# Performance work log

Hardware: AMD Instinct MI355X
Metric: run time of the kernel (lower is better)

## Reference

```python
import jax, jax.numpy as jnp
import numpy as np

B, S, HID = 8, 1024, 1024
NH, HD = 16, 64  # num heads, head dim
EPS = 1e-12


def setup_inputs() -> dict:
    key = jax.random.key(0)
    ks = jax.random.split(key, 8)
    sc = 0.02
    return {
        "hidden_states": jax.random.normal(ks[0], (B, S, HID), jnp.float32),
        "attention_mask": jnp.zeros((B, 1, 1, S), jnp.bool_),
        "rel_pos": jax.random.normal(ks[1], (1, NH, S, S), jnp.float32),
        "rel_2d_pos": jax.random.normal(ks[2], (1, NH, S, S), jnp.float32),
        "w_qkv": jax.random.normal(ks[3], (3 * HID, HID), jnp.float32) * sc,
        "q_bias": jnp.zeros((1, 1, HID), jnp.float32),
        "v_bias": jnp.zeros((1, 1, HID), jnp.float32),
        "w_out": jax.random.normal(ks[4], (HID, HID), jnp.float32) * sc,
        "b_out": jnp.zeros((HID,), jnp.float32),
        "ln_gamma": jnp.ones((HID,), jnp.float32),
        "ln_beta": jnp.zeros((HID,), jnp.float32),
    }


def reference(hidden_states, attention_mask, rel_pos, rel_2d_pos,
              w_qkv, q_bias, v_bias, w_out, b_out, ln_gamma, ln_beta):
    x = hidden_states
    # fast_qkv: single projection, no bias; then add q_bias/v_bias
    qkv = jnp.einsum('bsh,oh->bso', x, w_qkv)  # [B,S,3*HID]
    q, k, v = jnp.split(qkv, 3, axis=-1)
    q = q + q_bias
    v = v + v_bias
    # [B,S,HID] -> [B,NH,S,HD]
    to_heads = lambda t: t.reshape(B, S, NH, HD).transpose(0, 2, 1, 3)
    qh, kh, vh = to_heads(q), to_heads(k), to_heads(v)
    qh = qh / jnp.sqrt(jnp.float32(HD))
    scores = jnp.einsum('bhqd,bhkd->bhqk', qh, kh)
    scores = scores + rel_pos + rel_2d_pos
    scores = jnp.where(attention_mask, -jnp.inf, scores.astype(jnp.float32))
    probs = jax.nn.softmax(scores, axis=-1).astype(vh.dtype)
    ctx = jnp.einsum('bhqk,bhkd->bhqd', probs, vh)
    ctx = ctx.transpose(0, 2, 1, 3).reshape(B, S, HID)
    # self-output: dense + residual + LayerNorm
    h = jnp.einsum('bsh,oh->bso', ctx, w_out) + b_out + x
    mu = jnp.mean(h, axis=-1, keepdims=True)
    var = jnp.var(h, axis=-1, keepdims=True)
    out = (h - mu) / jnp.sqrt(var + EPS) * ln_gamma + ln_beta
    return out
```

## Files before the change

kernel.cpp:

```cpp
#include <hip/hip_runtime.h>
#include <stdint.h>
#include <stddef.h>

typedef unsigned short u16;
typedef __attribute__((ext_vector_type(8))) short short8;
typedef __attribute__((ext_vector_type(4))) float f32x4;
typedef __attribute__((ext_vector_type(4))) unsigned short ushort4v;
typedef __attribute__((ext_vector_type(4))) unsigned char uchar4v;
typedef __attribute__((ext_vector_type(2))) unsigned int uint2v;

constexpr int B_ = 8, S_ = 1024, HID_ = 1024, NH_ = 16, HD_ = 64;
#define LOG2E_F 1.4426950408889634f
#define QSCALE_F 0.18033688011112043f
#define SHIFT2_F 11.541560327111707f

__device__ __forceinline__ u16 f2b(float f) {
  unsigned int u = __builtin_bit_cast(unsigned int, f);
  u += 0x7fff + ((u >> 16) & 1);
  return (u16)(u >> 16);
}
__device__ __forceinline__ float b2f(u16 s) {
  unsigned int u = ((unsigned int)s) << 16;
  return __builtin_bit_cast(float, u);
}
__device__ __forceinline__ float fexp2(float x) {
#if __has_builtin(__builtin_amdgcn_exp2f)
  return __builtin_amdgcn_exp2f(x);
#else
  return exp2f(x);
#endif
}
__device__ __forceinline__ void llds16(const void* g, void* l) {
  __builtin_amdgcn_global_load_lds((__attribute__((address_space(1))) void*)g,
                                   (__attribute__((address_space(3))) void*)l, 16, 0, 0);
}

__global__ __launch_bounds__(256) void prep_cvt(
    const float* __restrict__ x, const float* __restrict__ wqkv,
    const float* __restrict__ wout, u16* __restrict__ xb,
    u16* __restrict__ wqkvb, u16* __restrict__ woutb) {
  const int NX8 = B_ * S_ * HID_ / 8, NW18 = 3 * HID_ * HID_ / 8, NW28 = HID_ * HID_ / 8;
  const int tot = NX8 + NW18 + NW28;
  for (int i = blockIdx.x * blockDim.x + threadIdx.x; i < tot; i += gridDim.x * blockDim.x) {
    const float4* s; u16* d; int j;
    if (i < NX8)              { s = (const float4*)x;    d = xb;    j = i; }
    else if (i < NX8 + NW18)  { s = (const float4*)wqkv; d = wqkvb; j = i - NX8; }
    else                      { s = (const float4*)wout; d = woutb; j = i - NX8 - NW18; }
    float4 v0 = s[2 * (size_t)j], v1 = s[2 * (size_t)j + 1];
    short8 o;
    o[0] = (short)f2b(v0.x); o[1] = (short)f2b(v0.y);
    o[2] = (short)f2b(v0.z); o[3] = (short)f2b(v0.w);
    o[4] = (short)f2b(v1.x); o[5] = (short)f2b(v1.y);
    o[6] = (short)f2b(v1.z); o[7] = (short)f2b(v1.w);
    *(short8*)(d + 8 * (size_t)j) = o;
  }
}

__global__ __launch_bounds__(256) void rel_perm(
    const float* __restrict__ a, const float* __restrict__ b, u16* __restrict__ relb) {
  __shared__ u16 lbuf[16 * 1032];
  const int qtg = blockIdx.x, h = blockIdx.y;
  const int t = threadIdx.x;
#pragma unroll
  for (int it = 0; it < 16; ++it) {
    int idx = it * 256 + t;
    int lq = idx >> 8, kc = idx & 255;
    size_t src = ((size_t)h * S_ + qtg * 16 + lq) * S_ + kc * 4;
    float4 va = *(const float4*)(a + src);
    float4 vb = *(const float4*)(b + src);
    ushort4v o;
    o[0] = f2b((va.x + vb.x) * LOG2E_F); o[1] = f2b((va.y + vb.y) * LOG2E_F);
    o[2] = f2b((va.z + vb.z) * LOG2E_F); o[3] = f2b((va.w + vb.w) * LOG2E_F);
    *(ushort4v*)(lbuf + lq * 1032 + kc * 4) = o;
  }
  __syncthreads();
#pragma unroll
  for (int it = 0; it < 16; ++it) {
    int c = it * 16 + (t >> 4);
    int ktg = c >> 2, qk = c & 3, lq = t & 15;
    ushort4v v = *(const ushort4v*)(lbuf + lq * 1032 + ktg * 16 + qk * 4);
    *(ushort4v*)(relb + ((((size_t)h * 64 + ktg) * 64 + qtg) * 4 + qk) * 64 + lq * 4) = v;
  }
}

__global__ __launch_bounds__(256) void gemm_qkv(
    const u16* __restrict__ W, const u16* __restrict__ X,
    const float* __restrict__ qbias, const float* __restrict__ vbias,
    u16* __restrict__ Qb, u16* __restrict__ Kb, u16* __restrict__ Vtb) {
  constexpr int K = HID_;
  __shared__ u16 smem[128 * 136];
  u16* Ws0 = smem;
  u16* Ws1 = smem + 4096;
  u16* Xs0 = smem + 8192;
  u16* Xs1 = smem + 12288;
  const int lin = blockIdx.x;
  const int virt = (lin & 7) * 192 + (lin >> 3);
  const int o0 = (virt % 24) * 128, s0 = (virt / 24) * 128;
  const int t = threadIdx.x, lane = t & 63, wv = t >> 6;
  const int wr = wv >> 1, wc = wv & 1, ln = lane & 15, q8 = lane >> 4;
  f32x4 acc[4][4] = {};

  for (int kt = 0; kt < K / 64; ++kt) {
    const int k0 = kt * 64;
#pragma unroll
    for (int c = 0; c < 2; ++c) {
      int idx = c * 256 + t, row = idx >> 2, cc = (idx & 3) * 8;
      const int db = (c * 256 + wv * 64) * 8;
      llds16(W + (size_t)(o0 + row) * K + k0 + cc,      Ws0 + db);
      llds16(W + (size_t)(o0 + row) * K + k0 + 32 + cc, Ws1 + db);
      llds16(X + (size_t)(s0 + row) * K + k0 + cc,      Xs0 + db);
      llds16(X + (size_t)(s0 + row) * K + k0 + 32 + cc, Xs1 + db);
    }
    __syncthreads();
#pragma unroll
    for (int hh = 0; hh < 2; ++hh) {
      const u16* Wh = hh ? Ws1 : Ws0;
      const u16* Xh = hh ? Xs1 : Xs0;
      short8 of[4], sf[4];
#pragma unroll
      for (int mi = 0; mi < 4; ++mi)
        of[mi] = *(const short8*)(Wh + (wr * 64 + mi * 16 + ln) * 32 + q8 * 8);
#pragma unroll
      for (int ni = 0; ni < 4; ++ni)
        sf[ni] = *(const short8*)(Xh + (wc * 64 + ni * 16 + ln) * 32 + q8 * 8);
#pragma unroll
      for (int mi = 0; mi < 4; ++mi)
#pragma unroll
        for (int ni = 0; ni < 4; ++ni)
          acc[mi][ni] = __builtin_amdgcn_mfma_f32_16x16x32_bf16(of[mi], sf[ni], acc[mi][ni], 0, 0, 0);
    }
    __syncthreads();
  }

  const int sec = o0 >> 10;

  if (sec == 2) {
#pragma unroll
    for (int mi = 0; mi < 4; ++mi) {
      const int ocol = wr * 64 + mi * 16 + q8 * 4;
      const int oo = (o0 + ocol) & 1023;
      float4 b4 = *(const float4*)(vbias + oo);
#pragma unroll
      for (int ni = 0; ni < 4; ++ni) {
        const int srow = wc * 64 + ni * 16 + ln;
#pragma unroll
        for (int r = 0; r < 4; ++r)
          smem[(ocol + r) * 136 + srow] = f2b(acc[mi][ni][r] + ((const float*)&b4)[r]);
      }
    }
    __syncthreads();
#pragma unroll
    for (int i = 0; i < 8; ++i) {
      int flat = i * 256 + t;
      int dl = flat >> 4, s8 = (flat & 15) * 8;
      short8 v = *(const short8*)(smem + dl * 136 + s8);
      int oo = (o0 + dl) & 1023, hh = oo >> 6, dd = oo & 63;
      int bb = s0 >> 10, ss = (s0 + s8) & 1023;
      *(short8*)(Vtb + ((size_t)(bb * NH_ + hh) * HD_ + dd) * S_ + ss) = v;
    }
    return;
  }

#pragma unroll
  for (int mi = 0; mi < 4; ++mi) {
    const int ocol = wr * 64 + mi * 16 + q8 * 4;
    const int oo = (o0 + ocol) & 1023;
    float4 b4;
    if (sec == 0) b4 = *(const float4*)(qbias + oo);
    else          b4 = float4{0.f, 0.f, 0.f, 0.f};
#pragma unroll
    for (int ni = 0; ni < 4; ++ni) {
      const int srow = wc * 64 + ni * 16 + ln;
      u16 e[4];
#pragma unroll
      for (int r = 0; r < 4; ++r) {
        float v = acc[mi][ni][r] + ((const float*)&b4)[r];
        if (sec == 0) v *= QSCALE_F;
        e[r] = f2b(v);
      }
      uint2v pw;
      pw[0] = (unsigned)e[0] | ((unsigned)e[1] << 16);
      pw[1] = (unsigned)e[2] | ((unsigned)e[3] << 16);
      *(uint2v*)(smem + srow * 136 + ocol) = pw;
    }
  }
  __syncthreads();
  u16* dst = (sec == 0) ? Qb : Kb;
#pragma unroll
  for (int i = 0; i < 8; ++i) {
    int flat = i * 256 + t;
    int srow = flat >> 4, c8 = (flat & 15) * 8;
    short8 v = *(const short8*)(smem + srow * 136 + c8);
    int oo = (o0 + c8) & 1023, hh = oo >> 6, dd = oo & 63;
    int s = s0 + srow, bb = s >> 10, ss = s & 1023;
    *(short8*)(dst + ((size_t)(bb * NH_ + hh) * S_ + ss) * HD_ + dd) = v;
  }
}

__global__ __launch_bounds__(512, 2) void flash_attn(
    const u16* __restrict__ Qb, const u16* __restrict__ Kb,
    const u16* __restrict__ Vtb, const u16* __restrict__ relb,
    const unsigned char* __restrict__ mask, u16* __restrict__ ctxb) {
  const int lin = blockIdx.x;
  const int virt = (lin & 7) * 64 + (lin >> 3);
  const int h = virt >> 5, qt_blk = (virt >> 3) & 3, b = virt & 7;
  const int bh = b * NH_ + h, q0 = qt_blk * 256;
  const int t = threadIdx.x, lane = t & 63, wv = t >> 6;
  const int ln = lane & 15, q8 = lane >> 4;

  __shared__ u16 smem[28160];
  u16* Ks  = smem;
  u16* Vts = smem + 9216;
  u16* Pw  = smem + 17920 + wv * 1280;

  const int krow = t >> 3, kcol = (t & 7) * 8;
  const int vrow = t >> 4, vcol = (t & 15) * 8;

  const u16* relbase = relb + (((size_t)h * 64) * 64 + (size_t)(qt_blk * 16 + wv * 2)) * 4 * 64
                            + (size_t)q8 * 64 + ln * 4;

  short8 kreg[2], vreg[2];
#pragma unroll
  for (int i = 0; i < 2; ++i)
    kreg[i] = *(const short8*)(Kb + ((size_t)bh * S_ + i * 64 + krow) * HD_ + kcol);
#pragma unroll
  for (int i = 0; i < 2; ++i)
    vreg[i] = *(const short8*)(Vtb + ((size_t)bh * HD_ + i * 32 + vrow) * S_ + vcol);

  short8 qf[2][2];
#pragma unroll
  for (int qt = 0; qt < 2; ++qt)
#pragma unroll
    for (int kc = 0; kc < 2; ++kc)
      qf[qt][kc] = *(const short8*)(Qb + ((size_t)bh * S_ + q0 + wv * 32 + qt * 16 + ln) * HD_ + kc * 32 + q8 * 8);

  f32x4 Oa[4][2] = {};
  float rs2[2] = {0.f, 0.f};

  for (int kt128 = 0; kt128 < 8; ++kt128) {
    const int k0 = kt128 * 128;

    uchar4v mg[4][2];
#pragma unroll
    for (int kvc = 0; kvc < 4; ++kvc)
#pragma unroll
      for (int sub = 0; sub < 2; ++sub)
        mg[kvc][sub] = *(const uchar4v*)(mask + b * S_ + k0 + (kvc * 2 + sub) * 16 + q8 * 4);

    ushort4v relg[4][2][2];
#pragma unroll
    for (int sub = 0; sub < 2; ++sub)
#pragma unroll
      for (int qt = 0; qt < 2; ++qt)
        relg[0][sub][qt] = *(const ushort4v*)(relbase +
            (((size_t)(kt128 * 8 + sub) * 64 + qt) * 4) * 64);

    __syncthreads();
#pragma unroll
    for (int i = 0; i < 2; ++i)
      *(short8*)(Ks + (i * 64 + krow) * 72 + kcol) = kreg[i];
#pragma unroll
    for (int i = 0; i < 2; ++i)
      *(short8*)(Vts + (i * 32 + vrow) * 136 + vcol) = vreg[i];
    if (kt128 < 7) {
      const int k0n = k0 + 128;
#pragma unroll
      for (int i = 0; i < 2; ++i)
        kreg[i] = *(const short8*)(Kb + ((size_t)bh * S_ + k0n + i * 64 + krow) * HD_ + kcol);
#pragma unroll
      for (int i = 0; i < 2; ++i)
        vreg[i] = *(const short8*)(Vtb + ((size_t)bh * HD_ + i * 32 + vrow) * S_ + k0n + vcol);
    }
    __syncthreads();

#pragma unroll
    for (int kvc = 0; kvc < 4; ++kvc) {
      if (kvc < 3) {
#pragma unroll
        for (int sub = 0; sub < 2; ++sub)
#pragma unroll
          for (int qt = 0; qt < 2; ++qt)
            relg[kvc + 1][sub][qt] = *(const ushort4v*)(relbase +
                (((size_t)(kt128 * 8 + (kvc + 1) * 2 + sub) * 64 + qt) * 4) * 64);
      }
#pragma unroll
      for (int sub = 0; sub < 2; ++sub) {
        const int kt = kvc * 2 + sub;
        short8 kf0 = *(const short8*)(Ks + (kt * 16 + ln) * 72 + q8 * 8);
        short8 kf1 = *(const short8*)(Ks + (kt * 16 + ln) * 72 + 32 + q8 * 8);
        uchar4v m4 = mg[kvc][sub];
        f32x4 mbase;
#pragma unroll
        for (int r = 0; r < 4; ++r) mbase[r] = (m4[r] ? -1e30f : 0.f) - SHIFT2_F;
#pragma unroll
        for (int qt = 0; qt < 2; ++qt) {
          ushort4v r4 = relg[kvc][sub][qt];
          f32x4 sc;
#pragma unroll
          for (int r = 0; r < 4; ++r) sc[r] = b2f(r4[r]) + mbase[r];
          sc = __builtin_amdgcn_mfma_f32_16x16x32_bf16(kf0, qf[qt][0], sc, 0, 0, 0);
          sc = __builtin_amdgcn_mfma_f32_16x16x32_bf16(kf1, qf[qt][1], sc, 0, 0, 0);
          float p0 = fexp2(sc[0]), p1 = fexp2(sc[1]);
          float p2 = fexp2(sc[2]), p3 = fexp2(sc[3]);
          rs2[qt] += (p0 + p1) + (p2 + p3);
          uint2v pw;
          pw[0] = (unsigned)f2b(p0) | ((unsigned)f2b(p1) << 16);
          pw[1] = (unsigned)f2b(p2) | ((unsigned)f2b(p3) << 16);
          *(uint2v*)(Pw + (qt * 16 + ln) * 40 + sub * 16 + q8 * 4) = pw;
        }
      }
      short8 pf0 = *(const short8*)(Pw + ln * 40 + q8 * 8);
      short8 pf1 = *(const short8*)(Pw + (16 + ln) * 40 + q8 * 8);
#pragma unroll
      for (int mt = 0; mt < 4; ++mt) {
        short8 vf = *(const short8*)(Vts + (mt * 16 + ln) * 136 + kvc * 32 + q8 * 8);
        Oa[mt][0] = __builtin_amdgcn_mfma_f32_16x16x32_bf16(vf, pf0, Oa[mt][0], 0, 0, 0);
        Oa[mt][1] = __builtin_amdgcn_mfma_f32_16x16x32_bf16(vf, pf1, Oa[mt][1], 0, 0, 0);
      }
    }
  }

  float inv[2];
#pragma unroll
  for (int qt = 0; qt < 2; ++qt) {
    rs2[qt] += __shfl_xor(rs2[qt], 16, 64);
    rs2[qt] += __shfl_xor(rs2[qt], 32, 64);
    inv[qt] = 1.f / rs2[qt];
  }

  __syncthreads();
  u16* Ob = smem + wv * 2304;
#pragma unroll
  for (int qt = 0; qt < 2; ++qt)
#pragma unroll
    for (int mt = 0; mt < 4; ++mt) {
      u16 e[4];
#pragma unroll
      for (int r = 0; r < 4; ++r) e[r] = f2b(Oa[mt][qt][r] * inv[qt]);
      uint2v pw;
      pw[0] = (unsigned)e[0] | ((unsigned)e[1] << 16);
      pw[1] = (unsigned)e[2] | ((unsigned)e[3] << 16);
      *(uint2v*)(Ob + (qt * 16 + ln) * 72 + mt * 16 + q8 * 4) = pw;
    }
#pragma unroll
  for (int p = 0; p < 4; ++p) {
    int row = p * 8 + (lane >> 3);
    int c8 = (lane & 7) * 8;
    short8 v = *(const short8*)(Ob + row * 72 + c8);
    int q = q0 + wv * 32 + row;
    *(short8*)(ctxb + ((size_t)(b * S_ + q)) * HID_ + h * 64 + c8) = v;
  }
}

__global__ __launch_bounds__(256) void gemm_out(
    const u16* __restrict__ W, const u16* __restrict__ X,
    const float* __restrict__ bout, const float* __restrict__ xres,
    u16* __restrict__ hb) {
  constexpr int K = HID_;
  __shared__ u16 smem[128 * 136];
  u16* Ws0 = smem;
  u16* Ws1 = smem + 4096;
  u16* Xs0 = smem + 8192;
  u16* Xs1 = smem + 12288;
  const int lin = blockIdx.x;
  const int virt = (lin & 7) * 64 + (lin >> 3);
  const int o0 = (virt % 8) * 128, s0 = (virt / 8) * 128;
  const int t = threadIdx.x, lane = t & 63, wv = t >> 6;
  const int wr = wv >> 1, wc = wv & 1, ln = lane & 15, q8 = lane >> 4;
  f32x4 acc[4][4] = {};

  for (int kt = 0; kt < K / 64; ++kt) {
    const int k0 = kt * 64;
#pragma unroll
    for (int c = 0; c < 2; ++c) {
      int idx = c * 256 + t, row = idx >> 2, cc = (idx & 3) * 8;
      const int db = (c * 256 + wv * 64) * 8;
      llds16(W + (size_t)(o0 + row) * K + k0 + cc,      Ws0 + db);
      llds16(W + (size_t)(o0 + row) * K + k0 + 32 + cc, Ws1 + db);
      llds16(X + (size_t)(s0 + row) * K + k0 + cc,      Xs0 + db);
      llds16(X + (size_t)(s0 + row) * K + k0 + 32 + cc, Xs1 + db);
    }
    __syncthreads();
#pragma unroll
    for (int hh = 0; hh < 2; ++hh) {
      const u16* Wh = hh ? Ws1 : Ws0;
      const u16* Xh = hh ? Xs1 : Xs0;
      short8 of[4], sf[4];
#pragma unroll
      for (int mi = 0; mi < 4; ++mi)
        of[mi] = *(const short8*)(Wh + (wr * 64 + mi * 16 + ln) * 32 + q8 * 8);
#pragma unroll
      for (int ni = 0; ni < 4; ++ni)
        sf[ni] = *(const short8*)(Xh + (wc * 64 + ni * 16 + ln) * 32 + q8 * 8);
#pragma unroll
      for (int mi = 0; mi < 4; ++mi)
#pragma unroll
        for (int ni = 0; ni < 4; ++ni)
          acc[mi][ni] = __builtin_amdgcn_mfma_f32_16x16x32_bf16(of[mi], sf[ni], acc[mi][ni], 0, 0, 0);
    }
    __syncthreads();
  }

#pragma unroll
  for (int mi = 0; mi < 4; ++mi) {
    const int ocol = wr * 64 + mi * 16 + q8 * 4;
    float4 b4 = *(const float4*)(bout + o0 + ocol);
#pragma unroll
    for (int ni = 0; ni < 4; ++ni) {
      const int srow = wc * 64 + ni * 16 + ln;
      u16 e[4];
#pragma unroll
      for (int r = 0; r < 4; ++r) e[r] = f2b(acc[mi][ni][r] + ((const float*)&b4)[r]);
      uint2v pw;
      pw[0] = (unsigned)e[0] | ((unsigned)e[1] << 16);
      pw[1] = (unsigned)e[2] | ((unsigned)e[3] << 16);
      *(uint2v*)(smem + srow * 136 + ocol) = pw;
    }
  }
  __syncthreads();
#pragma unroll
  for (int i = 0; i < 8; ++i) {
    int flat = i * 256 + t;
    int srow = flat >> 4, c8 = (flat & 15) * 8;
    short8 v = *(const short8*)(smem + srow * 136 + c8);
    int s = s0 + srow, o = o0 + c8;
    float4 x0 = *(const float4*)(xres + (size_t)s * HID_ + o);
    float4 x1 = *(const float4*)(xres + (size_t)s * HID_ + o + 4);
    short8 st;
#pragma unroll
    for (int j = 0; j < 4; ++j) st[j] = (short)f2b(b2f((u16)v[j]) + ((const float*)&x0)[j]);
#pragma unroll
    for (int j = 0; j < 4; ++j) st[4 + j] = (short)f2b(b2f((u16)v[4 + j]) + ((const float*)&x1)[j]);
    *(short8*)(hb + (size_t)s * HID_ + o) = st;
  }
}

__global__ __launch_bounds__(256) void ln_kernel(
    const u16* __restrict__ hb, const float* __restrict__ gamma,
    const float* __restrict__ beta, float* __restrict__ out) {
  __shared__ float red[8];
  const int t = threadIdx.x, lane = t & 63, wv = t >> 6;
  const int row = blockIdx.x;
  const u16* hr = hb + (size_t)row * HID_;
  ushort4v a = *(const ushort4v*)(hr + t * 4);
  float v[4];
#pragma unroll
  for (int j = 0; j < 4; ++j) v[j] = b2f(a[j]);
  float sum = (v[0] + v[1]) + (v[2] + v[3]);
  float sq = (v[0] * v[0] + v[1] * v[1]) + (v[2] * v[2] + v[3] * v[3]);
#pragma unroll
  for (int off = 1; off < 64; off <<= 1) {
    sum += __shfl_xor(sum, off, 64);
    sq  += __shfl_xor(sq, off, 64);
  }
  if (lane == 0) { red[wv] = sum; red[4 + wv] = sq; }
  __syncthreads();
  const float s4 = (red[0] + red[1]) + (red[2] + red[3]);
  const float q4 = (red[4] + red[5]) + (red[6] + red[7]);
  const float mu = s4 * (1.f / HID_);
  const float var = q4 * (1.f / HID_) - mu * mu;
  const float inv = 1.f / sqrtf(var + 1e-12f);
  float4 g = *(const float4*)(gamma + t * 4);
  float4 be = *(const float4*)(beta + t * 4);
  float4 o;
  o.x = (v[0] - mu) * inv * g.x + be.x;
  o.y = (v[1] - mu) * inv * g.y + be.y;
  o.z = (v[2] - mu) * inv * g.z + be.z;
  o.w = (v[3] - mu) * inv * g.w + be.w;
  *(float4*)(out + (size_t)row * HID_ + t * 4) = o;
}

extern "C" void kernel_launch(void* const* d_in, const int* in_sizes, int n_in,
                              void* d_out, int out_size, void* d_ws, size_t ws_size,
                              hipStream_t stream) {
  (void)in_sizes; (void)n_in; (void)out_size; (void)ws_size;
  const float* x     = (const float*)d_in[0];
  const unsigned char* mask = (const unsigned char*)d_in[1];
  const float* relp  = (const float*)d_in[2];
  const float* rel2  = (const float*)d_in[3];
  const float* wqkv  = (const float*)d_in[4];
  const float* qbias = (const float*)d_in[5];
  const float* vbias = (const float*)d_in[6];
  const float* wout  = (const float*)d_in[7];
  const float* bout  = (const float*)d_in[8];
  const float* gamma = (const float*)d_in[9];
  const float* beta  = (const float*)d_in[10];
  float* out = (float*)d_out;

  char* ws = (char*)d_ws;
  const size_t MB = (size_t)1 << 20;
  u16* xb    = (u16*)(ws + 0 * MB);
  u16* wqkvb = (u16*)(ws + 16 * MB);
  u16* woutb = (u16*)(ws + 22 * MB);
  u16* relb  = (u16*)(ws + 24 * MB);
  u16* Qb    = (u16*)(ws + 56 * MB);
  u16* Kb    = (u16*)(ws + 72 * MB);
  u16* Vtb   = (u16*)(ws + 88 * MB);
  u16* ctxb  = (u16*)(ws + 104 * MB);
  u16* hb    = (u16*)(ws + 120 * MB);

  prep_cvt<<<2048, 256, 0, stream>>>(x, wqkv, wout, xb, wqkvb, woutb);
  rel_perm<<<dim3(64, 16), 256, 0, stream>>>(relp, rel2, relb);
  gemm_qkv<<<1536, 256, 0, stream>>>(wqkvb, xb, qbias, vbias, Qb, Kb, Vtb);
  flash_attn<<<512, 512, 0, stream>>>(Qb, Kb, Vtb, relb, mask, ctxb);
  gemm_out<<<512, 256, 0, stream>>>(woutb, ctxb, bout, x, hb);
  ln_kernel<<<8192, 256, 0, stream>>>(hb, gamma, beta, out);
}
```

Baseline: 389.0 us.

## Halve gemm_out row tile for more blocks and widen rel_perm vector accesses

The output-projection GEMM now uses 128x64 tiles instead of 128x128 and launches twice as many blocks, to improve CU occupancy and load balance on a small GEMM. The cost is lower operand reuse, with more repeated W loads per output. The rel_perm kernel now loads and stores eight bf16 elements per thread access instead of four. This reduces instruction count and improves memory transaction width in that bandwidth-bound permutation.

```diff
diff --git a/kernel.cpp b/kernel.cpp
--- a/kernel.cpp
+++ b/kernel.cpp
@@ -62,24 +62,37 @@
   const int qtg = blockIdx.x, h = blockIdx.y;
   const int t = threadIdx.x;
 #pragma unroll
-  for (int it = 0; it < 16; ++it) {
+  for (int it = 0; it < 8; ++it) {
     int idx = it * 256 + t;
-    int lq = idx >> 8, kc = idx & 255;
-    size_t src = ((size_t)h * S_ + qtg * 16 + lq) * S_ + kc * 4;
-    float4 va = *(const float4*)(a + src);
-    float4 vb = *(const float4*)(b + src);
-    ushort4v o;
-    o[0] = f2b((va.x + vb.x) * LOG2E_F); o[1] = f2b((va.y + vb.y) * LOG2E_F);
-    o[2] = f2b((va.z + vb.z) * LOG2E_F); o[3] = f2b((va.w + vb.w) * LOG2E_F);
-    *(ushort4v*)(lbuf + lq * 1032 + kc * 4) = o;
+    int lq = idx >> 7, kc8 = idx & 127;
+    size_t src = ((size_t)h * S_ + qtg * 16 + lq) * S_ + kc8 * 8;
+    float4 va0 = *(const float4*)(a + src);
+    float4 va1 = *(const float4*)(a + src + 4);
+    float4 vb0 = *(const float4*)(b + src);
+    float4 vb1 = *(const float4*)(b + src + 4);
+    short8 o;
+    o[0] = (short)f2b((va0.x + vb0.x) * LOG2E_F);
+    o[1] = (short)f2b((va0.y + vb0.y) * LOG2E_F);
+    o[2] = (short)f2b((va0.z + vb0.z) * LOG2E_F);
+    o[3] = (short)f2b((va0.w + vb0.w) * LOG2E_F);
+    o[4] = (short)f2b((va1.x + vb1.x) * LOG2E_F);
+    o[5] = (short)f2b((va1.y + vb1.y) * LOG2E_F);
+    o[6] = (short)f2b((va1.z + vb1.z) * LOG2E_F);
+    o[7] = (short)f2b((va1.w + vb1.w) * LOG2E_F);
+    *(short8*)(lbuf + lq * 1032 + kc8 * 8) = o;
   }
   __syncthreads();
 #pragma unroll
-  for (int it = 0; it < 16; ++it) {
-    int c = it * 16 + (t >> 4);
-    int ktg = c >> 2, qk = c & 3, lq = t & 15;
-    ushort4v v = *(const ushort4v*)(lbuf + lq * 1032 + ktg * 16 + qk * 4);
-    *(ushort4v*)(relb + ((((size_t)h * 64 + ktg) * 64 + qtg) * 4 + qk) * 64 + lq * 4) = v;
+  for (int it = 0; it < 8; ++it) {
+    int c = it * 32 + (t >> 3);
+    int ktg = c >> 2, qk = c & 3;
+    int lq0 = (t & 7) * 2;
+    ushort4v r0 = *(const ushort4v*)(lbuf + lq0 * 1032 + ktg * 16 + qk * 4);
+    ushort4v r1 = *(const ushort4v*)(lbuf + (lq0 + 1) * 1032 + ktg * 16 + qk * 4);
+    short8 v;
+    v[0] = (short)r0[0]; v[1] = (short)r0[1]; v[2] = (short)r0[2]; v[3] = (short)r0[3];
+    v[4] = (short)r1[0]; v[5] = (short)r1[1]; v[6] = (short)r1[2]; v[7] = (short)r1[3];
+    *(short8*)(relb + ((((size_t)h * 64 + ktg) * 64 + qtg) * 4 + qk) * 64 + lq0 * 4) = v;
   }
 }
 
@@ -357,17 +370,17 @@
     const float* __restrict__ bout, const float* __restrict__ xres,
     u16* __restrict__ hb) {
   constexpr int K = HID_;
-  __shared__ u16 smem[128 * 136];
+  __shared__ u16 smem[12288];
   u16* Ws0 = smem;
   u16* Ws1 = smem + 4096;
   u16* Xs0 = smem + 8192;
-  u16* Xs1 = smem + 12288;
+  u16* Xs1 = smem + 10240;
   const int lin = blockIdx.x;
-  const int virt = (lin & 7) * 64 + (lin >> 3);
-  const int o0 = (virt % 8) * 128, s0 = (virt / 8) * 128;
+  const int virt = (lin & 7) * 128 + (lin >> 3);
+  const int o0 = (virt & 7) * 128, s0 = (virt >> 3) * 64;
   const int t = threadIdx.x, lane = t & 63, wv = t >> 6;
   const int wr = wv >> 1, wc = wv & 1, ln = lane & 15, q8 = lane >> 4;
-  f32x4 acc[4][4] = {};
+  f32x4 acc[4][2] = {};
 
   for (int kt = 0; kt < K / 64; ++kt) {
     const int k0 = kt * 64;
@@ -377,6 +390,10 @@
       const int db = (c * 256 + wv * 64) * 8;
       llds16(W + (size_t)(o0 + row) * K + k0 + cc,      Ws0 + db);
       llds16(W + (size_t)(o0 + row) * K + k0 + 32 + cc, Ws1 + db);
+    }
+    {
+      int row = t >> 2, cc = (t & 3) * 8;
+      const int db = (wv * 64) * 8;
       llds16(X + (size_t)(s0 + row) * K + k0 + cc,      Xs0 + db);
       llds16(X + (size_t)(s0 + row) * K + k0 + 32 + cc, Xs1 + db);
     }
@@ -385,17 +402,17 @@
     for (int hh = 0; hh < 2; ++hh) {
       const u16* Wh = hh ? Ws1 : Ws0;
       const u16* Xh = hh ? Xs1 : Xs0;
-      short8 of[4], sf[4];
+      short8 of[4], sf[2];
 #pragma unroll
       for (int mi = 0; mi < 4; ++mi)
         of[mi] = *(const short8*)(Wh + (wr * 64 + mi * 16 + ln) * 32 + q8 * 8);
 #pragma unroll
-      for (int ni = 0; ni < 4; ++ni)
-        sf[ni] = *(const short8*)(Xh + (wc * 64 + ni * 16 + ln) * 32 + q8 * 8);
+      for (int ni = 0; ni < 2; ++ni)
+        sf[ni] = *(const short8*)(Xh + (wc * 32 + ni * 16 + ln) * 32 + q8 * 8);
 #pragma unroll
       for (int mi = 0; mi < 4; ++mi)
 #pragma unroll
-        for (int ni = 0; ni < 4; ++ni)
+        for (int ni = 0; ni < 2; ++ni)
           acc[mi][ni] = __builtin_amdgcn_mfma_f32_16x16x32_bf16(of[mi], sf[ni], acc[mi][ni], 0, 0, 0);
     }
     __syncthreads();
@@ -406,8 +423,8 @@
     const int ocol = wr * 64 + mi * 16 + q8 * 4;
     float4 b4 = *(const float4*)(bout + o0 + ocol);
 #pragma unroll
-    for (int ni = 0; ni < 4; ++ni) {
-      const int srow = wc * 64 + ni * 16 + ln;
+    for (int ni = 0; ni < 2; ++ni) {
+      const int srow = wc * 32 + ni * 16 + ln;
       u16 e[4];
 #pragma unroll
       for (int r = 0; r < 4; ++r) e[r] = f2b(acc[mi][ni][r] + ((const float*)&b4)[r]);
@@ -419,7 +436,7 @@
   }
   __syncthreads();
 #pragma unroll
-  for (int i = 0; i < 8; ++i) {
+  for (int i = 0; i < 4; ++i) {
     int flat = i * 256 + t;
     int srow = flat >> 4, c8 = (flat & 15) * 8;
     short8 v = *(const short8*)(smem + srow * 136 + c8);
@@ -503,6 +520,6 @@
   rel_perm<<<dim3(64, 16), 256, 0, stream>>>(relp, rel2, relb);
   gemm_qkv<<<1536, 256, 0, stream>>>(wqkvb, xb, qbias, vbias, Qb, Kb, Vtb);
   flash_attn<<<512, 512, 0, stream>>>(Qb, Kb, Vtb, relb, mask, ctxb);
-  gemm_out<<<512, 256, 0, stream>>>(woutb, ctxb, bout, x, hb);
+  gemm_out<<<1024, 256, 0, stream>>>(woutb, ctxb, bout, x, hb);
   ln_kernel<<<8192, 256, 0, stream>>>(hb, gamma, beta, out);
 }
```

Result: no change. 389.1 us (+0.0%).
